# Kernel tuning notes

Hardware: AMD Instinct MI355X
Metric: run time of the kernel (lower is better)

## Reference

```python
import jax, jax.numpy as jnp
import numpy as np


def _wn_dense_relu(x, v, g, bias):
    # torch weight_norm over dim=0: w[h,:] = g[h] * v[h,:] / ||v[h,:]||
    w = g[:, None] * v / jnp.linalg.norm(v, axis=1, keepdims=True)  # (hid, inp)
    return jax.nn.relu(jnp.einsum('bld,hd->blh', x, w) + bias)


def _masked_softmax(scores, mask, axis):
    # additive large-negative masking, numerically stable softmax
    return jax.nn.softmax(scores + jnp.where(mask > 0, 0.0, -1e9), axis=axis)


def setup_inputs() -> dict:
    key = jax.random.key(0)
    ks = jax.random.split(key, 6)
    B, La, Lb, D, H = 8, 2048, 2048, 256, 256
    return {
        'a': jax.random.normal(ks[0], (B, La, D), dtype=jnp.float32),
        'b': jax.random.normal(ks[1], (B, Lb, D), dtype=jnp.float32),
        'mask_a': jax.random.randint(ks[2], (B, La), 0, 2, dtype=jnp.int32),
        'mask_b': jax.random.randint(ks[3], (B, Lb), 0, 2, dtype=jnp.int32),
        'a_v': jax.random.normal(ks[4], (H, D), dtype=jnp.float32) * (2.0 / D) ** 0.5,
        'a_g': jnp.ones((H,), dtype=jnp.float32),
        'a_bias': jnp.zeros((H,), dtype=jnp.float32),
        'b_v': jax.random.normal(ks[5], (H, D), dtype=jnp.float32) * (2.0 / D) ** 0.5,
        'b_g': jnp.ones((H,), dtype=jnp.float32),
        'b_bias': jnp.zeros((H,), dtype=jnp.float32),
        'tau': jnp.asarray((1.0 / H) ** 0.5, dtype=jnp.float32),
    }


def reference(a, b, mask_a, mask_b, a_v, a_g, a_bias, b_v, b_g, b_bias, tau):
    ha = _wn_dense_relu(a, a_v, a_g, a_bias)                 # (B, La, H)
    hb = _wn_dense_relu(b, b_v, b_g, b_bias)                 # (B, Lb, H)
    attn = jnp.einsum('bih,bjh->bij', ha, hb) * tau          # (B, La, Lb)
    weight_a = _masked_softmax(attn, mask_a[:, :, None], axis=1)  # softmax over La
    weight_b = _masked_softmax(attn, mask_b[:, None, :], axis=2)  # softmax over Lb
    align_a = jnp.einsum('bij,bjd->bid', weight_b, b)        # (B, La, D)
    align_b = jnp.einsum('bij,bid->bjd', weight_a, a)        # (B, Lb, D)
    return align_a, align_b
```

## Files before the change

kernel.cpp:

```cpp
#include <hip/hip_runtime.h>
#include <hip/hip_bf16.h>
#include <stdint.h>

#define B_   8
#define L_   2048
#define D_   256
#define H_   256
#define TJ   64
#define NT   (L_/TJ)
#define BM   128
#define LOG2E 1.4426950408889634f

typedef short bf16x8 __attribute__((ext_vector_type(8)));
typedef short bf16x4 __attribute__((ext_vector_type(4)));
typedef float f32x4  __attribute__((ext_vector_type(4)));

#define MFMA(a,b,c) __builtin_amdgcn_mfma_f32_16x16x32_bf16(a,b,c,0,0,0)
#define EX2(x) __builtin_amdgcn_exp2f(x)

typedef unsigned int u32;
__device__ __forceinline__ void gload_lds16(const void* g, void* l){
  __builtin_amdgcn_global_load_lds((const __attribute__((address_space(1))) u32*)g,
                                   (__attribute__((address_space(3))) u32*)l, 16, 0, 0);
}

__device__ __forceinline__ unsigned short f2bf(float f){
  __hip_bfloat16 h = __float2bfloat16(f);
  unsigned short us;
  __builtin_memcpy(&us, &h, 2);
  return us;
}

__device__ __forceinline__ void bar_lgkm(){
  asm volatile("s_waitcnt lgkmcnt(0)" ::: "memory");
  __builtin_amdgcn_s_barrier();
  __builtin_amdgcn_sched_barrier(0);
}
__device__ __forceinline__ void bar_all(){
  asm volatile("s_waitcnt vmcnt(0) lgkmcnt(0)" ::: "memory");
  __builtin_amdgcn_s_barrier();
  __builtin_amdgcn_sched_barrier(0);
}

__global__ __launch_bounds__(256) void wnorm_kernel(const float* __restrict__ av,
      const float* __restrict__ ag, const float* __restrict__ bv,
      const float* __restrict__ bg, unsigned short* __restrict__ wa,
      unsigned short* __restrict__ wb){
  int sel = blockIdx.y;
  const float* v = sel ? bv : av;
  const float* g = sel ? bg : ag;
  unsigned short* w = sel ? wb : wa;
  int h = blockIdx.x;
  int d = threadIdx.x;
  float x = v[h*D_ + d];
  float sq = x*x;
  for (int off = 32; off; off >>= 1) sq += __shfl_down(sq, off, 64);
  __shared__ float red[4];
  int lane = threadIdx.x & 63, wid = threadIdx.x >> 6;
  if (lane == 0) red[wid] = sq;
  __syncthreads();
  float tot = red[0] + red[1] + red[2] + red[3];
  float scale = g[h] / sqrtf(tot);
  w[h*D_ + d] = f2bf(x * scale);
}

__global__ __launch_bounds__(256) void hgemm_kernel(const float* __restrict__ a,
      const float* __restrict__ b, const unsigned short* __restrict__ wa,
      const unsigned short* __restrict__ wb, const float* __restrict__ a_bias,
      const float* __restrict__ b_bias, const float* __restrict__ tau_ptr,
      unsigned short* __restrict__ ha, unsigned short* __restrict__ hb,
      unsigned short* __restrict__ aT, unsigned short* __restrict__ bT){
  __shared__ __align__(16) unsigned short xtile[256*68];
  int sel = blockIdx.y;
  const float* x = sel ? b : a;
  const unsigned short* w = sel ? wb : wa;
  const float* bias = sel ? b_bias : a_bias;
  unsigned short* hx = sel ? hb : ha;
  unsigned short* xT = sel ? bT : aT;
  float scale = sel ? 1.0f : tau_ptr[0] * LOG2E;
  int m0 = blockIdx.x * 64;
  int bz = m0 / L_, l0 = m0 % L_;
  int tid = threadIdx.x;
  int lane = tid & 63, wid = tid >> 6;
  int p = lane & 15, q = lane >> 4;
  int row = m0 + wid*16 + p;
  unsigned short* xtw = xtile + (q*8)*68 + (wid*16 + p);
  f32x4 acc[16] = {};
  for (int kk = 0; kk < 8; kk++){
    const float* ap = x + (size_t)row * 256 + kk*32 + q*8;
    f32x4 a0 = *(const f32x4*)ap;
    f32x4 a1 = *(const f32x4*)(ap + 4);
    bf16x8 af;
    af[0]=(short)f2bf(a0[0]); af[1]=(short)f2bf(a0[1]); af[2]=(short)f2bf(a0[2]); af[3]=(short)f2bf(a0[3]);
    af[4]=(short)f2bf(a1[0]); af[5]=(short)f2bf(a1[1]); af[6]=(short)f2bf(a1[2]); af[7]=(short)f2bf(a1[3]);
    #pragma unroll
    for (int e = 0; e < 8; e++)
      xtw[(kk*32 + e)*68] = (unsigned short)af[e];
    #pragma unroll
    for (int n = 0; n < 16; n++){
      bf16x8 bfr = *(const bf16x8*)(w + (size_t)(n*16 + p) * 256 + kk*32 + q*8);
      acc[n] = MFMA(af, bfr, acc[n]);
    }
  }
  #pragma unroll
  for (int n = 0; n < 16; n++){
    float bv = bias[n*16 + p];
    #pragma unroll
    for (int r = 0; r < 4; r++){
      int orow = m0 + wid*16 + q*4 + r;
      float vv = acc[n][r] + bv;
      vv = vv > 0.f ? vv : 0.f;
      hx[(size_t)orow * 256 + n*16 + p] = f2bf(vv * scale);
    }
  }
  __syncthreads();
  #pragma unroll
  for (int it = 0; it < 16; it++){
    int d = it*16 + (tid >> 4);
    int c = (tid & 15) * 4;
    bf16x4 v = *(const bf16x4*)(&xtile[d*68 + c]);
    *(bf16x4*)(xT + ((size_t)bz*D_ + d)*L_ + l0 + c) = v;
  }
}

__global__ __launch_bounds__(512, 2) void flash_kernel(
    const unsigned short* __restrict__ ha, const unsigned short* __restrict__ hb,
    const unsigned short* __restrict__ aT, const unsigned short* __restrict__ bT,
    const int* __restrict__ mask_a, const int* __restrict__ mask_b,
    float* __restrict__ out)
{
  __shared__ __align__(16) unsigned short HBT[2][64][256];
  __shared__ __align__(16) unsigned short VTL[2][256][64];
  __shared__ __align__(16) unsigned short WT[4][32][64];
  __shared__ float MST[8][32];
  __shared__ float SST[8][32];
  __shared__ float MSKL[2048];

  const int bid = blockIdx.x;
  const int s   = bid & 15;
  const int dir = s >> 3;
  const int bz  = s & 7;
  const int i0  = (bid >> 4) * BM;
  const int tid = threadIdx.x;
  const int lane = tid & 63;
  const int wid  = tid >> 6;
  const int wr = wid >> 1, wc = wid & 1;
  const int p = lane & 15, q = lane >> 4;

  const unsigned short* hA = dir ? hb : ha;
  const unsigned short* hB = dir ? ha : hb;
  const unsigned short* vT = dir ? aT : bT;
  const int* mask = dir ? mask_a : mask_b;
  float* outp = out + ((size_t)dir * B_ + bz) * L_ * D_;

  const unsigned short* hAp = hA + (size_t)bz * L_ * H_;
  const unsigned short* hBp = hB + (size_t)bz * L_ * H_;
  const unsigned short* vTp = vT + (size_t)bz * D_ * L_;
  const int* mp = mask + bz * L_;

  const int hb_r0 = wid*2 + (lane >> 5);
  const int hb_s  = lane & 31;
  const int vt_r0 = wid*8 + (lane >> 3);
  const int vt_s  = lane & 7;

  bf16x8 af[2][8];
  #pragma unroll
  for (int g = 0; g < 2; ++g)
    #pragma unroll
    for (int kk = 0; kk < 8; ++kk)
      af[g][kk] = *(const bf16x8*)(hAp + (size_t)(i0 + wr*32 + g*16 + p) * H_ + kk*32 + q*8);

  #pragma unroll
  for (int i = 0; i < 4; ++i){
    int idx = tid + i*512;
    MSKL[idx] = (mp[idx] > 0) ? 0.f : -1e9f;
  }

  f32x4 acc[2][8];
  #pragma unroll
  for (int g = 0; g < 2; ++g)
    #pragma unroll
    for (int n = 0; n < 8; ++n) acc[g][n] = (f32x4){0.f,0.f,0.f,0.f};
  float m_run[2], s_run[2];
  m_run[0] = m_run[1] = -1e30f;
  s_run[0] = s_run[1] = 0.f;

  #define STAGE(bb, jj0) do {                                                     \
    _Pragma("unroll")                                                             \
    for (int k = 0; k < 4; ++k){                                                  \
      int rr = k*16 + hb_r0;                                                      \
      int sp = hb_s ^ (rr & 7);                                                   \
      gload_lds16(hBp + (size_t)((jj0) + rr) * H_ + sp*8,                         \
                  &HBT[bb][0][0] + (k*8192 + wid*1024)/2);                        \
    }                                                                             \
    _Pragma("unroll")                                                             \
    for (int k = 0; k < 4; ++k){                                                  \
      int rr = k*64 + vt_r0;                                                      \
      int sp = vt_s ^ (rr & 7);                                                   \
      gload_lds16(vTp + (size_t)rr * L_ + (jj0) + sp*8,                           \
                  &VTL[bb][0][0] + (k*8192 + wid*1024)/2);                        \
    }                                                                             \
  } while(0)

  STAGE(0, 0);
  bar_all();

  for (int jt = 0; jt < NT; ++jt){
    const int j0 = jt * TJ;
    const int cur = jt & 1;
    if (jt + 1 < NT) STAGE(cur ^ 1, j0 + TJ);

    f32x4 accp[2][2];
    #pragma unroll
    for (int g = 0; g < 2; ++g)
      #pragma unroll
      for (int cg = 0; cg < 2; ++cg) accp[g][cg] = (f32x4){0.f,0.f,0.f,0.f};
    __builtin_amdgcn_s_setprio(1);
    #pragma unroll
    for (int kk = 0; kk < 8; ++kk){
      const int rb = wc*32 + p;
      const int sp = ((kk*4 + q) ^ (p & 7)) * 8;
      bf16x8 b0 = *(const bf16x8*)(&HBT[cur][0][0] + rb*256 + sp);
      bf16x8 b1 = *(const bf16x8*)(&HBT[cur][0][0] + (rb+16)*256 + sp);
      accp[0][0] = MFMA(b0, af[0][kk], accp[0][0]);
      accp[1][0] = MFMA(b0, af[1][kk], accp[1][0]);
      accp[0][1] = MFMA(b1, af[0][kk], accp[0][1]);
      accp[1][1] = MFMA(b1, af[1][kk], accp[1][1]);
    }
    __builtin_amdgcn_s_setprio(0);

    f32x4 mm0 = *(const f32x4*)(&MSKL[j0 + wc*32 + q*4]);
    f32x4 mm1 = *(const f32x4*)(&MSKL[j0 + wc*32 + 16 + q*4]);
    #pragma unroll
    for (int g = 0; g < 2; ++g)
      #pragma unroll
      for (int r = 0; r < 4; ++r){
        accp[g][0][r] += mm0[r];
        accp[g][1][r] += mm1[r];
      }

    float tmax[2];
    #pragma unroll
    for (int g = 0; g < 2; ++g){
      float t0 = fmaxf(fmaxf(accp[g][0][0], accp[g][0][1]),
                       fmaxf(accp[g][0][2], accp[g][0][3]));
      float t1 = fmaxf(fmaxf(accp[g][1][0], accp[g][1][1]),
                       fmaxf(accp[g][1][2], accp[g][1][3]));
      tmax[g] = fmaxf(t0, t1);
      tmax[g] = fmaxf(tmax[g], __shfl_xor(tmax[g], 16, 64));
      tmax[g] = fmaxf(tmax[g], __shfl_xor(tmax[g], 32, 64));
    }

    if (q == 0){
      MST[wid][p]      = tmax[0];
      MST[wid][16 + p] = tmax[1];
    }
    bar_lgkm();

    float pm[2];
    pm[0] = fmaxf(tmax[0], MST[wid ^ 1][p]);
    pm[1] = fmaxf(tmax[1], MST[wid ^ 1][16 + p]);

    int need = (pm[0] > m_run[0] + 11.54f) || (pm[1] > m_run[1] + 11.54f);
    if (__any(need)){
      float fsc[2];
      #pragma unroll
      for (int g = 0; g < 2; ++g){
        float mn = fmaxf(m_run[g], pm[g]);
        fsc[g] = EX2(m_run[g] - mn);
        s_run[g] *= fsc[g];
        m_run[g] = mn;
      }
      float fT[2][4];
      #pragma unroll
      for (int g = 0; g < 2; ++g)
        #pragma unroll
        for (int r = 0; r < 4; ++r)
          fT[g][r] = __shfl(fsc[g], (lane & 48) | (q*4 + r), 64);
      #pragma unroll
      for (int g = 0; g < 2; ++g)
        #pragma unroll
        for (int n = 0; n < 8; ++n)
          #pragma unroll
          for (int r = 0; r < 4; ++r)
            acc[g][n][r] *= fT[g][r];
    }

    #pragma unroll
    for (int g = 0; g < 2; ++g){
      #pragma unroll
      for (int cg = 0; cg < 2; ++cg){
        float w0 = EX2(accp[g][cg][0] - m_run[g]);
        float w1 = EX2(accp[g][cg][1] - m_run[g]);
        float w2 = EX2(accp[g][cg][2] - m_run[g]);
        float w3 = EX2(accp[g][cg][3] - m_run[g]);
        s_run[g] += (w0 + w1) + (w2 + w3);
        uint2 wv;
        wv.x = (u32)f2bf(w0) | ((u32)f2bf(w1) << 16);
        wv.y = (u32)f2bf(w2) | ((u32)f2bf(w3) << 16);
        int row = g*16 + p;
        int sl  = (wc*4 + cg*2 + (q>>1)) ^ (row & 7);
        *(uint2*)(&WT[wr][0][0] + row*64 + (sl<<3) + ((q&1)<<2)) = wv;
      }
    }
    bar_lgkm();

    bf16x8 wf[2][2];
    #pragma unroll
    for (int g = 0; g < 2; ++g)
      #pragma unroll
      for (int ks = 0; ks < 2; ++ks){
        int row = g*16 + p;
        wf[g][ks] = *(const bf16x8*)(&WT[wr][0][0] + row*64
                                     + ((((ks*4 + q) ^ (row & 7)))<<3));
      }

    __builtin_amdgcn_s_setprio(1);
    #pragma unroll
    for (int n = 0; n < 8; ++n){
      const int d = wc*128 + n*16 + p;
      #pragma unroll
      for (int ks = 0; ks < 2; ++ks){
        const int sp = ((ks*4 + q) ^ (p & 7)) * 8;
        bf16x8 vf = *(const bf16x8*)(&VTL[cur][0][0] + d*64 + sp);
        acc[0][n] = MFMA(wf[0][ks], vf, acc[0][n]);
        acc[1][n] = MFMA(wf[1][ks], vf, acc[1][n]);
      }
    }
    __builtin_amdgcn_s_setprio(0);

    bar_all();
  }
  #undef STAGE

  #pragma unroll
  for (int g = 0; g < 2; ++g){
    s_run[g] += __shfl_xor(s_run[g], 16, 64);
    s_run[g] += __shfl_xor(s_run[g], 32, 64);
  }
  if (q == 0){
    SST[wid][p]      = s_run[0];
    SST[wid][16 + p] = s_run[1];
  }
  __syncthreads();
  float invS[2][4];
  #pragma unroll
  for (int g = 0; g < 2; ++g)
    #pragma unroll
    for (int r = 0; r < 4; ++r){
      int idx = g*16 + q*4 + r;
      invS[g][r] = 1.0f / (SST[wr*2][idx] + SST[wr*2 + 1][idx]);
    }

  #pragma unroll
  for (int g = 0; g < 2; ++g)
    #pragma unroll
    for (int n = 0; n < 8; ++n)
      #pragma unroll
      for (int r = 0; r < 4; ++r){
        int row = i0 + wr*32 + g*16 + q*4 + r;
        outp[(size_t)row * D_ + wc*128 + n*16 + p] = acc[g][n][r] * invS[g][r];
      }
}

extern "C" void kernel_launch(void* const* d_in, const int* in_sizes, int n_in,
                              void* d_out, int out_size, void* d_ws, size_t ws_size,
                              hipStream_t stream) {
  const float* a      = (const float*)d_in[0];
  const float* b      = (const float*)d_in[1];
  const int*   mask_a = (const int*)d_in[2];
  const int*   mask_b = (const int*)d_in[3];
  const float* a_v    = (const float*)d_in[4];
  const float* a_g    = (const float*)d_in[5];
  const float* a_bias = (const float*)d_in[6];
  const float* b_v    = (const float*)d_in[7];
  const float* b_g    = (const float*)d_in[8];
  const float* b_bias = (const float*)d_in[9];
  const float* tau    = (const float*)d_in[10];

  float* out = (float*)d_out;

  char* ws = (char*)d_ws;
  const size_t SZ_W  = (size_t)H_ * D_ * 2;
  const size_t SZ_H  = (size_t)B_ * L_ * H_ * 2;
  unsigned short* wa = (unsigned short*)(ws);
  unsigned short* wb = (unsigned short*)(ws + SZ_W);
  unsigned short* ha = (unsigned short*)(ws + 2*SZ_W);
  unsigned short* hb = (unsigned short*)(ws + 2*SZ_W + SZ_H);
  unsigned short* aT = (unsigned short*)(ws + 2*SZ_W + 2*SZ_H);
  unsigned short* bT = (unsigned short*)(ws + 2*SZ_W + 3*SZ_H);
  size_t need = 2*SZ_W + 4*SZ_H;
  if (ws_size < need) return;

  wnorm_kernel<<<dim3(H_, 2), 256, 0, stream>>>(a_v, a_g, b_v, b_g, wa, wb);

  {
    dim3 g((B_*L_)/64, 2);
    hgemm_kernel<<<g, 256, 0, stream>>>(a, b, wa, wb, a_bias, b_bias, tau,
                                        ha, hb, aT, bT);
  }

  {
    flash_kernel<<<dim3((L_/BM) * B_ * 2), 512, 0, stream>>>(
        ha, hb, aT, bT, mask_a, mask_b, out);
  }
}
```

Measured before the change: 144.2 us.

## Replace online softmax max with precomputed Cauchy-Schwarz norm bound

Computes per-row L2 norms of the projected activations in the projection GEMM, plus a per-batch max norm via atomicMax. The attention kernel then uses the product of these norms as a fixed upper bound on each row's scores instead of tracking a running max. This removes the per-tile max reduction, the shared-memory exchange and barrier, and the conditional accumulator rescaling from the inner loop. The trade-off is possible underflow or precision loss when the bound greatly exceeds the true row maximum.

After: 228.0 us. 58.1% more time.

```diff
diff --git a/kernel.cpp b/kernel.cpp
--- a/kernel.cpp
+++ b/kernel.cpp
@@ -45,8 +45,9 @@
 __global__ __launch_bounds__(256) void wnorm_kernel(const float* __restrict__ av,
       const float* __restrict__ ag, const float* __restrict__ bv,
       const float* __restrict__ bg, unsigned short* __restrict__ wa,
-      unsigned short* __restrict__ wb){
+      unsigned short* __restrict__ wb, float* __restrict__ maxn){
   int sel = blockIdx.y;
+  if (blockIdx.x == 0 && threadIdx.x < 8) maxn[sel*8 + threadIdx.x] = 0.f;
   const float* v = sel ? bv : av;
   const float* g = sel ? bg : ag;
   unsigned short* w = sel ? wb : wa;
@@ -69,7 +70,9 @@
       const unsigned short* __restrict__ wb, const float* __restrict__ a_bias,
       const float* __restrict__ b_bias, const float* __restrict__ tau_ptr,
       unsigned short* __restrict__ ha, unsigned short* __restrict__ hb,
-      unsigned short* __restrict__ aT, unsigned short* __restrict__ bT){
+      unsigned short* __restrict__ aT, unsigned short* __restrict__ bT,
+      float* __restrict__ rn_a, float* __restrict__ rn_b,
+      float* __restrict__ maxn){
   __shared__ __align__(16) unsigned short xtile[256*68];
   int sel = blockIdx.y;
   const float* x = sel ? b : a;
@@ -77,6 +80,7 @@
   const float* bias = sel ? b_bias : a_bias;
   unsigned short* hx = sel ? hb : ha;
   unsigned short* xT = sel ? bT : aT;
+  float* rn = sel ? rn_b : rn_a;
   float scale = sel ? 1.0f : tau_ptr[0] * LOG2E;
   int m0 = blockIdx.x * 64;
   int bz = m0 / L_, l0 = m0 % L_;
@@ -102,6 +106,7 @@
       acc[n] = MFMA(af, bfr, acc[n]);
     }
   }
+  float rs[4] = {0.f, 0.f, 0.f, 0.f};
   #pragma unroll
   for (int n = 0; n < 16; n++){
     float bv = bias[n*16 + p];
@@ -110,7 +115,23 @@
       int orow = m0 + wid*16 + q*4 + r;
       float vv = acc[n][r] + bv;
       vv = vv > 0.f ? vv : 0.f;
-      hx[(size_t)orow * 256 + n*16 + p] = f2bf(vv * scale);
+      float sv = vv * scale;
+      rs[r] += sv * sv;
+      hx[(size_t)orow * 256 + n*16 + p] = f2bf(sv);
+    }
+  }
+  #pragma unroll
+  for (int off = 1; off < 16; off <<= 1)
+    #pragma unroll
+    for (int r = 0; r < 4; r++)
+      rs[r] += __shfl_xor(rs[r], off, 64);
+  if (p == 0){
+    #pragma unroll
+    for (int r = 0; r < 4; r++){
+      int orow = m0 + wid*16 + q*4 + r;
+      float rv = sqrtf(rs[r]) * 1.01f;
+      rn[orow] = rv;
+      atomicMax((u32*)&maxn[sel*8 + bz], __float_as_uint(rv));
     }
   }
   __syncthreads();
@@ -127,12 +148,12 @@
     const unsigned short* __restrict__ ha, const unsigned short* __restrict__ hb,
     const unsigned short* __restrict__ aT, const unsigned short* __restrict__ bT,
     const int* __restrict__ mask_a, const int* __restrict__ mask_b,
-    float* __restrict__ out)
+    const float* __restrict__ rn_a, const float* __restrict__ rn_b,
+    const float* __restrict__ maxn, float* __restrict__ out)
 {
   __shared__ __align__(16) unsigned short HBT[2][64][256];
   __shared__ __align__(16) unsigned short VTL[2][256][64];
   __shared__ __align__(16) unsigned short WT[4][32][64];
-  __shared__ float MST[8][32];
   __shared__ float SST[8][32];
   __shared__ float MSKL[2048];
 
@@ -151,6 +172,8 @@
   const unsigned short* hB = dir ? ha : hb;
   const unsigned short* vT = dir ? aT : bT;
   const int* mask = dir ? mask_a : mask_b;
+  const float* rnA = dir ? rn_b : rn_a;
+  const float mxB  = maxn[(dir ^ 1)*8 + bz];
   float* outp = out + ((size_t)dir * B_ + bz) * L_ * D_;
 
   const unsigned short* hAp = hA + (size_t)bz * L_ * H_;
@@ -170,6 +193,11 @@
     for (int kk = 0; kk < 8; ++kk)
       af[g][kk] = *(const bf16x8*)(hAp + (size_t)(i0 + wr*32 + g*16 + p) * H_ + kk*32 + q*8);
 
+  float m_p[2];
+  #pragma unroll
+  for (int g = 0; g < 2; ++g)
+    m_p[g] = rnA[bz*L_ + i0 + wr*32 + g*16 + p] * mxB;
+
   #pragma unroll
   for (int i = 0; i < 4; ++i){
     int idx = tid + i*512;
@@ -181,8 +209,7 @@
   for (int g = 0; g < 2; ++g)
     #pragma unroll
     for (int n = 0; n < 8; ++n) acc[g][n] = (f32x4){0.f,0.f,0.f,0.f};
-  float m_run[2], s_run[2];
-  m_run[0] = m_run[1] = -1e30f;
+  float s_run[2];
   s_run[0] = s_run[1] = 0.f;
 
   #define STAGE(bb, jj0) do {                                                     \
@@ -231,69 +258,16 @@
 
     f32x4 mm0 = *(const f32x4*)(&MSKL[j0 + wc*32 + q*4]);
     f32x4 mm1 = *(const f32x4*)(&MSKL[j0 + wc*32 + 16 + q*4]);
-    #pragma unroll
-    for (int g = 0; g < 2; ++g)
-      #pragma unroll
-      for (int r = 0; r < 4; ++r){
-        accp[g][0][r] += mm0[r];
-        accp[g][1][r] += mm1[r];
-      }
-
-    float tmax[2];
+
     #pragma unroll
     for (int g = 0; g < 2; ++g){
-      float t0 = fmaxf(fmaxf(accp[g][0][0], accp[g][0][1]),
-                       fmaxf(accp[g][0][2], accp[g][0][3]));
-      float t1 = fmaxf(fmaxf(accp[g][1][0], accp[g][1][1]),
-                       fmaxf(accp[g][1][2], accp[g][1][3]));
-      tmax[g] = fmaxf(t0, t1);
-      tmax[g] = fmaxf(tmax[g], __shfl_xor(tmax[g], 16, 64));
-      tmax[g] = fmaxf(tmax[g], __shfl_xor(tmax[g], 32, 64));
-    }
-
-    if (q == 0){
-      MST[wid][p]      = tmax[0];
-      MST[wid][16 + p] = tmax[1];
-    }
-    bar_lgkm();
-
-    float pm[2];
-    pm[0] = fmaxf(tmax[0], MST[wid ^ 1][p]);
-    pm[1] = fmaxf(tmax[1], MST[wid ^ 1][16 + p]);
-
-    int need = (pm[0] > m_run[0] + 11.54f) || (pm[1] > m_run[1] + 11.54f);
-    if (__any(need)){
-      float fsc[2];
-      #pragma unroll
-      for (int g = 0; g < 2; ++g){
-        float mn = fmaxf(m_run[g], pm[g]);
-        fsc[g] = EX2(m_run[g] - mn);
-        s_run[g] *= fsc[g];
-        m_run[g] = mn;
-      }
-      float fT[2][4];
-      #pragma unroll
-      for (int g = 0; g < 2; ++g)
-        #pragma unroll
-        for (int r = 0; r < 4; ++r)
-          fT[g][r] = __shfl(fsc[g], (lane & 48) | (q*4 + r), 64);
-      #pragma unroll
-      for (int g = 0; g < 2; ++g)
-        #pragma unroll
-        for (int n = 0; n < 8; ++n)
-          #pragma unroll
-          for (int r = 0; r < 4; ++r)
-            acc[g][n][r] *= fT[g][r];
-    }
-
-    #pragma unroll
-    for (int g = 0; g < 2; ++g){
       #pragma unroll
       for (int cg = 0; cg < 2; ++cg){
-        float w0 = EX2(accp[g][cg][0] - m_run[g]);
-        float w1 = EX2(accp[g][cg][1] - m_run[g]);
-        float w2 = EX2(accp[g][cg][2] - m_run[g]);
-        float w3 = EX2(accp[g][cg][3] - m_run[g]);
+        const f32x4 mm = cg ? mm1 : mm0;
+        float w0 = EX2(accp[g][cg][0] + mm[0] - m_p[g]);
+        float w1 = EX2(accp[g][cg][1] + mm[1] - m_p[g]);
+        float w2 = EX2(accp[g][cg][2] + mm[2] - m_p[g]);
+        float w3 = EX2(accp[g][cg][3] + mm[3] - m_p[g]);
         s_run[g] += (w0 + w1) + (w2 + w3);
         uint2 wv;
         wv.x = (u32)f2bf(w0) | ((u32)f2bf(w1) << 16);
@@ -333,11 +307,10 @@
   }
   #undef STAGE
 
-  #pragma unroll
-  for (int g = 0; g < 2; ++g){
-    s_run[g] += __shfl_xor(s_run[g], 16, 64);
-    s_run[g] += __shfl_xor(s_run[g], 32, 64);
-  }
+  s_run[0] += __shfl_xor(s_run[0], 16, 64);
+  s_run[0] += __shfl_xor(s_run[0], 32, 64);
+  s_run[1] += __shfl_xor(s_run[1], 16, 64);
+  s_run[1] += __shfl_xor(s_run[1], 32, 64);
   if (q == 0){
     SST[wid][p]      = s_run[0];
     SST[wid][16 + p] = s_run[1];
@@ -389,19 +362,22 @@
   unsigned short* hb = (unsigned short*)(ws + 2*SZ_W + SZ_H);
   unsigned short* aT = (unsigned short*)(ws + 2*SZ_W + 2*SZ_H);
   unsigned short* bT = (unsigned short*)(ws + 2*SZ_W + 3*SZ_H);
-  size_t need = 2*SZ_W + 4*SZ_H;
+  float* rn_a = (float*)(ws + 2*SZ_W + 4*SZ_H);
+  float* rn_b = rn_a + (size_t)B_ * L_;
+  float* maxn = rn_b + (size_t)B_ * L_;
+  size_t need = 2*SZ_W + 4*SZ_H + 2*(size_t)B_*L_*4 + 64;
   if (ws_size < need) return;
 
-  wnorm_kernel<<<dim3(H_, 2), 256, 0, stream>>>(a_v, a_g, b_v, b_g, wa, wb);
+  wnorm_kernel<<<dim3(H_, 2), 256, 0, stream>>>(a_v, a_g, b_v, b_g, wa, wb, maxn);
 
   {
     dim3 g((B_*L_)/64, 2);
     hgemm_kernel<<<g, 256, 0, stream>>>(a, b, wa, wb, a_bias, b_bias, tau,
-                                        ha, hb, aT, bT);
+                                        ha, hb, aT, bT, rn_a, rn_b, maxn);
   }
 
   {
     flash_kernel<<<dim3((L_/BM) * B_ * 2), 512, 0, stream>>>(
-        ha, hb, aT, bT, mask_a, mask_b, out);
-  }
-}
+        ha, hb, aT, bT, mask_a, mask_b, rn_a, rn_b, maxn, out);
+  }
+}
```
